# Kernel optimization log

Measured on AMD Instinct MI355X. Metric: run time of the kernel, lower is better.

## Reference

```python
import jax, jax.numpy as jnp
import numpy as np

N = 500_000       # nodes
E = 8_000_000     # edges (avg degree 16)
IN_DIM = 16       # node_in_dim
HID = 32          # DCRNN hidden (hard-coded in RecurrentGCN)
OUT_DIM = 8       # node_out_dim


def setup_inputs() -> dict:
    key = jax.random.key(0)
    ks = jax.random.split(key, 12)
    scale_g = 1.0 / np.sqrt(IN_DIM + HID)  # glorot-ish for DConv weights
    scale_l = 1.0 / np.sqrt(HID)
    return {
        "x": jax.random.normal(ks[0], (N, IN_DIM), jnp.float32),
        "edge_index": jax.random.randint(ks[1], (2, E), 0, N, jnp.int32),
        "edge_weight": jax.random.uniform(ks[2], (E,), jnp.float32),
        "h": jnp.zeros((N, HID), jnp.float32),
        # DConv weights: original shape (2, K=1, in, out); K=1 -> store (2, in, out)
        "w_z": jax.random.normal(ks[3], (2, IN_DIM + HID, HID), jnp.float32) * scale_g,
        "b_z": jnp.zeros((HID,), jnp.float32),
        "w_r": jax.random.normal(ks[4], (2, IN_DIM + HID, HID), jnp.float32) * scale_g,
        "b_r": jnp.zeros((HID,), jnp.float32),
        "w_h": jax.random.normal(ks[5], (2, IN_DIM + HID, HID), jnp.float32) * scale_g,
        "b_h": jnp.zeros((HID,), jnp.float32),
        "w_lin": jax.random.normal(ks[6], (HID, OUT_DIM), jnp.float32) * scale_l,
        "b_lin": jnp.zeros((OUT_DIM,), jnp.float32),
    }


def _dconv_k1(xh, w, b):
    # DConv with K=1: only the Chebyshev k=0 term survives:
    #   H = X @ W[0,0] + X @ W[1,0] + b  (out-diffusion + in-diffusion weights)
    # edge_index / edge_weight do not enter the math for K=1.
    return xh @ (w[0] + w[1]) + b


def reference(x, edge_index, edge_weight, h, w_z, b_z, w_r, b_r, w_h, b_h, w_lin, b_lin):
    # DCRNN GRU cell (h=None in torch -> zeros, supplied explicitly here)
    xh = jnp.concatenate([x, h], axis=1)                  # [N, IN+HID]
    z = jax.nn.sigmoid(_dconv_k1(xh, w_z, b_z))           # update gate [N, HID]
    r = jax.nn.sigmoid(_dconv_k1(xh, w_r, b_r))           # reset gate  [N, HID]
    xhr = jnp.concatenate([x, h * r], axis=1)             # [N, IN+HID]
    h_tilde = jnp.tanh(_dconv_k1(xhr, w_h, b_h))          # candidate   [N, HID]
    h_new = z * h + (1.0 - z) * h_tilde                   # [N, HID]
    out = jax.nn.relu(h_new) @ w_lin + b_lin              # [N, OUT_DIM]
    return (out, h_new)
```

## Files before the change

kernel.cpp:

```cpp
#include <hip/hip_runtime.h>


#define N_NODES 500000
#define IN_DIM  16
#define HID     32
#define OUT_DIM 8
#define XH      48
#define NTILES  31250
#define WROW    72

typedef unsigned int u32;
typedef unsigned short u16;
typedef __attribute__((ext_vector_type(8))) short bf16x8;
typedef __attribute__((ext_vector_type(4))) float f32x4;

static __device__ __forceinline__ float bfbits(u32 hi){ union{u32 x; float f;} t; t.x=hi; return t.f; }
static __device__ __forceinline__ float bflo(u32 u){ return bfbits(u<<16); }
static __device__ __forceinline__ float bfhi(u32 u){ return bfbits(u & 0xffff0000u); }
static __device__ __forceinline__ float bf2f(u16 s){ return bfbits(((u32)s)<<16); }
static __device__ __forceinline__ float u2f(u32 u){ union{u32 x; float f;} t; t.x=u; return t.f; }
static __device__ __forceinline__ u32 f2u(float f){ union{float f;u32 x;} t; t.f=f; return t.x; }
static __device__ __forceinline__ u32 cvtpk(float a, float b){
    u32 r; asm("v_cvt_pk_bf16_f32 %0, %1, %2" : "=v"(r) : "v"(a), "v"(b)); return r;
}
static __device__ __forceinline__ u16 f2bf(float f){
    union{float f;u32 x;} t; t.f=f; u32 x=t.x;
    return (u16)((x + 0x7fffu + ((x>>16)&1u)) >> 16);
}
static __device__ __forceinline__ float sigm(float a){
    return 1.f / (1.f + __expf(-a));
}
static __device__ __forceinline__ float tanh_(float a){
    float e = __expf(-2.f * fabsf(a));
    float t = (1.f - e) / (1.f + e);
    return __builtin_copysignf(t, a);
}

#define LFENCE() asm volatile("s_waitcnt lgkmcnt(0)" ::: "memory")
#define MFMA16(a,b,c) __builtin_amdgcn_mfma_f32_16x16x32_bf16(a,b,c,0,0,0)

static __device__ __forceinline__ float ldf(const void* p, int i, bool F32){
    return F32 ? ((const float*)p)[i] : bf2f(((const u16*)p)[i]);
}
static __device__ __forceinline__ float wsum(const void* wp, int k, int c, bool F32){
    int i0 = k*HID + c;
    return ldf(wp, i0, F32) + ldf(wp, XH*HID + i0, F32);
}
static __device__ __forceinline__ char* stgp(char* base, int row, int off){
    return base + row*128 + (off ^ ((row & 7) << 4));
}

__global__ __launch_bounds__(256)
void rgcn_kernel(const void* __restrict__ xp_,
                 const void* __restrict__ hp_,
                 const void* __restrict__ wz_, const void* __restrict__ bz_,
                 const void* __restrict__ wr_, const void* __restrict__ br_,
                 const void* __restrict__ wh_, const void* __restrict__ bh_,
                 const void* __restrict__ wl_, const void* __restrict__ bl_,
                 void* __restrict__ dout_)
{
    __shared__ u16 sW[3][32*WROW];
    __shared__ u16 sStage[4][16*64];
    __shared__ int sF32;

    const int tid = threadIdx.x;

    if (tid < 64) {
        const u32* xw = (const u32*)xp_;
        int bad = 0;
#pragma unroll
        for (int q = 0; q < 2; q++) {
            float lo = bflo(xw[tid*2 + q]);
            if (!(fabsf(lo) <= 1e6f)) bad = 1;
        }
        unsigned long long m = __ballot(bad);
        if (tid == 0) sF32 = (m != 0ull) ? 1 : 0;
    }
    __syncthreads();
    const bool F32 = (sF32 != 0);

    {
        const void* wsrc[3] = { wz_, wr_, wh_ };
#pragma unroll
        for (int m = 0; m < 3; m++) {
            u32* dst = (u32*)sW[m];
            for (int o = tid; o < 32*(WROW/2); o += 256) {
                int c = o / (WROW/2), kk = o - c*(WROW/2);
                int k0 = 2*kk, k1 = 2*kk + 1;
                float v0 = (k0 < XH) ? wsum(wsrc[m], k0, c, F32) : 0.f;
                float v1 = (k1 < XH) ? wsum(wsrc[m], k1, c, F32) : 0.f;
                dst[o] = cvtpk(v0, v1);
            }
        }
    }
    __syncthreads();

    const int lane = tid & 63, wv = tid >> 6;
    const int c16 = lane & 15, g = lane >> 4;
    const int row4 = lane >> 2, q4 = lane & 3;
    char* stage = (char*)sStage[wv];

    char* pXw = stgp(stage, row4, q4*8);
    char* pHw = stgp(stage, row4, 32 + q4*16);
    char* pA0 = stgp(stage, c16, 16*g);
    char* pA1 = stgp(stage, c16, 64 + 16*g);
    char* pPairH[4]; char* pPairR[4];
#pragma unroll
    for (int rr = 0; rr < 4; rr++) {
        int nl = g*4 + rr;
        pPairH[rr] = stgp(stage, nl, 32 + 4*c16);
        pPairR[rr] = stgp(stage, nl, 4*c16);
    }

    {
        uint2 z2; z2.x = 0u; z2.y = 0u;
        *(uint2*)stgp(stage, row4, 96 + q4*8) = z2;
    }

    float bzv[2], brv[2], bhv[2];
#pragma unroll
    for (int tt = 0; tt < 2; tt++) {
        bzv[tt] = ldf(bz_, 2*c16 + tt, F32);
        brv[tt] = ldf(br_, 2*c16 + tt, F32);
        bhv[tt] = ldf(bh_, 2*c16 + tt, F32);
    }
    float blv = (c16 < OUT_DIM) ? ldf(bl_, c16, F32) : 0.f;

    bf16x8 Bz[2][2], Br[2][2], Bh[2][2], Bl;
#pragma unroll
    for (int kt = 0; kt < 2; kt++) {
#pragma unroll
        for (int tt = 0; tt < 2; tt++) {
            int boff = (2*c16 + tt)*(WROW*2) + (kt*32 + g*8)*2;
            Bz[kt][tt] = *(const bf16x8*)((const char*)sW[0] + boff);
            Br[kt][tt] = *(const bf16x8*)((const char*)sW[1] + boff);
            Bh[kt][tt] = *(const bf16x8*)((const char*)sW[2] + boff);
        }
    }
    {
        union { u16 us[8]; bf16x8 v; } ul;
#pragma unroll
        for (int e = 0; e < 8; e++) {
            int k = g*8 + e;
            float v = (c16 < OUT_DIM) ? ldf(wl_, k*OUT_DIM + c16, F32) : 0.f;
            ul.us[e] = f2bf(v);
        }
        Bl = ul.v;
    }

    float* outF = (float*)dout_;
    float* hnF  = outF + (size_t)N_NODES * OUT_DIM;
    u16*   outB = (u16*)dout_;
    u16*   hnB  = outB + (size_t)N_NODES * OUT_DIM;

    const int wid = blockIdx.x*4 + wv;
    const int nw  = gridDim.x*4;

    float4 pfx, pfh0, pfh1;
#define PLOAD(TT) do { \
        size_t nbp = (size_t)(TT) * 16; \
        if (F32) { \
            const float* xb = (const float*)xp_ + nbp*IN_DIM; \
            pfx  = *(const float4*)(xb + row4*IN_DIM + q4*4); \
            const float* hb = (const float*)hp_ + nbp*HID; \
            pfh0 = *(const float4*)(hb + row4*HID + q4*8); \
            pfh1 = *(const float4*)(hb + row4*HID + q4*8 + 4); \
        } else { \
            const u16* xb = (const u16*)xp_ + nbp*IN_DIM; \
            uint2 xv = *(const uint2*)(xb + row4*IN_DIM + q4*4); \
            pfx.x = u2f(xv.x); pfx.y = u2f(xv.y); \
            const u16* hb = (const u16*)hp_ + nbp*HID; \
            uint4 hv = *(const uint4*)(hb + row4*HID + q4*8); \
            pfh0.x = u2f(hv.x); pfh0.y = u2f(hv.y); pfh0.z = u2f(hv.z); pfh0.w = u2f(hv.w); \
        } \
    } while (0)

    if (wid < NTILES) PLOAD(wid);

    for (int t = wid; t < NTILES; t += nw) {
        const size_t nb = (size_t)t * 16;

        if (F32) {
            uint2 xp2; xp2.x = cvtpk(pfx.x, pfx.y); xp2.y = cvtpk(pfx.z, pfx.w);
            *(uint2*)pXw = xp2;
            uint4 hp4; hp4.x = cvtpk(pfh0.x, pfh0.y); hp4.y = cvtpk(pfh0.z, pfh0.w);
            hp4.z = cvtpk(pfh1.x, pfh1.y); hp4.w = cvtpk(pfh1.z, pfh1.w);
            *(uint4*)pHw = hp4;
        } else {
            uint2 xp2; xp2.x = f2u(pfx.x); xp2.y = f2u(pfx.y);
            *(uint2*)pXw = xp2;
            uint4 hp4; hp4.x = f2u(pfh0.x); hp4.y = f2u(pfh0.y);
            hp4.z = f2u(pfh0.z); hp4.w = f2u(pfh0.w);
            *(uint4*)pHw = hp4;
        }

        {
            int tn = t + nw;
            if (tn < NTILES) PLOAD(tn);
        }
        LFENCE();

        bf16x8 a0 = *(const bf16x8*)pA0;
        bf16x8 a1 = *(const bf16x8*)pA1;
        u32 hwp[4];
#pragma unroll
        for (int rr = 0; rr < 4; rr++) hwp[rr] = *(const u32*)pPairH[rr];

        f32x4 accZ[2], accR[2];
#pragma unroll
        for (int tt = 0; tt < 2; tt++) {
            f32x4 az; az[0]=bzv[tt]; az[1]=bzv[tt]; az[2]=bzv[tt]; az[3]=bzv[tt];
            az = MFMA16(a0, Bz[0][tt], az);
            az = MFMA16(a1, Bz[1][tt], az);
            accZ[tt] = az;
            f32x4 ar; ar[0]=brv[tt]; ar[1]=brv[tt]; ar[2]=brv[tt]; ar[3]=brv[tt];
            ar = MFMA16(a0, Br[0][tt], ar);
            ar = MFMA16(a1, Br[1][tt], ar);
            accR[tt] = ar;
        }

        float z0a[4], z1a[4], hv0[4], hv1[4];
#pragma unroll
        for (int rr = 0; rr < 4; rr++) {
            float h0 = bflo(hwp[rr]), h1 = bfhi(hwp[rr]);
            hv0[rr] = h0; hv1[rr] = h1;
            float z0 = sigm(accZ[0][rr]), z1 = sigm(accZ[1][rr]);
            z0a[rr] = z0; z1a[rr] = z1;
            float r0 = sigm(accR[0][rr]), r1 = sigm(accR[1][rr]);
            *(u32*)pPairH[rr] = cvtpk(h0*r0, h1*r1);
        }
        LFENCE();

        bf16x8 b0 = *(const bf16x8*)pA0;
        bf16x8 b1 = *(const bf16x8*)pA1;
        f32x4 accH[2];
#pragma unroll
        for (int tt = 0; tt < 2; tt++) {
            f32x4 ah; ah[0]=bhv[tt]; ah[1]=bhv[tt]; ah[2]=bhv[tt]; ah[3]=bhv[tt];
            ah = MFMA16(b0, Bh[0][tt], ah);
            ah = MFMA16(b1, Bh[1][tt], ah);
            accH[tt] = ah;
        }

#pragma unroll
        for (int rr = 0; rr < 4; rr++) {
            int nl = g*4 + rr;
            float t0 = tanh_(accH[0][rr]), t1 = tanh_(accH[1][rr]);
            float n0 = t0 + z0a[rr]*(hv0[rr] - t0);
            float n1 = t1 + z1a[rr]*(hv1[rr] - t1);
            *(u32*)pPairR[rr] = cvtpk(fmaxf(n0, 0.f), fmaxf(n1, 0.f));
            if (F32) {
                float2 st; st.x = n0; st.y = n1;
                *(float2*)(hnF + (nb + nl)*HID + 2*c16) = st;
            } else {
                *(u32*)(hnB + (nb + nl)*HID + 2*c16) = cvtpk(n0, n1);
            }
        }
        LFENCE();

        bf16x8 a3 = *(const bf16x8*)pA0;
        f32x4 accO; accO[0]=blv; accO[1]=blv; accO[2]=blv; accO[3]=blv;
        accO = MFMA16(a3, Bl, accO);
        if (c16 < OUT_DIM) {
            if (F32) {
#pragma unroll
                for (int rr = 0; rr < 4; rr++)
                    outF[(nb + g*4 + rr)*OUT_DIM + c16] = accO[rr];
            } else {
#pragma unroll
                for (int rr = 0; rr < 4; rr++)
                    outB[(nb + g*4 + rr)*OUT_DIM + c16] = (u16)(cvtpk(accO[rr], accO[rr]) & 0xffffu);
            }
        }
    }
#undef PLOAD
}

extern "C" void kernel_launch(void* const* d_in, const int* in_sizes, int n_in,
                              void* d_out, int out_size, void* d_ws, size_t ws_size,
                              hipStream_t stream) {
    const int block = 256;
    const int grid  = 2048;
    rgcn_kernel<<<grid, block, 0, stream>>>(
        d_in[0], d_in[3], d_in[4], d_in[5], d_in[6], d_in[7],
        d_in[8], d_in[9], d_in[10], d_in[11], d_out);
}
```

Baseline: 252.5 us.

## Transpose MFMA operands to drop LDS staging and use ds_bpermute shuffles

Result: slower. 262.2 us (+3.8%).

```diff
diff --git a/kernel.cpp b/kernel.cpp
--- a/kernel.cpp
+++ b/kernel.cpp
@@ -18,8 +18,6 @@
 static __device__ __forceinline__ float bflo(u32 u){ return bfbits(u<<16); }
 static __device__ __forceinline__ float bfhi(u32 u){ return bfbits(u & 0xffff0000u); }
 static __device__ __forceinline__ float bf2f(u16 s){ return bfbits(((u32)s)<<16); }
-static __device__ __forceinline__ float u2f(u32 u){ union{u32 x; float f;} t; t.x=u; return t.f; }
-static __device__ __forceinline__ u32 f2u(float f){ union{float f;u32 x;} t; t.f=f; return t.x; }
 static __device__ __forceinline__ u32 cvtpk(float a, float b){
     u32 r; asm("v_cvt_pk_bf16_f32 %0, %1, %2" : "=v"(r) : "v"(a), "v"(b)); return r;
 }
@@ -27,17 +25,18 @@
     union{float f;u32 x;} t; t.f=f; u32 x=t.x;
     return (u16)((x + 0x7fffu + ((x>>16)&1u)) >> 16);
 }
+static __device__ __forceinline__ float rcp_(float x){
+    float r; asm("v_rcp_f32 %0, %1" : "=v"(r) : "v"(x)); return r;
+}
 static __device__ __forceinline__ float sigm(float a){
-    return 1.f / (1.f + __expf(-a));
+    return rcp_(1.f + __expf(-a));
 }
 static __device__ __forceinline__ float tanh_(float a){
     float e = __expf(-2.f * fabsf(a));
-    float t = (1.f - e) / (1.f + e);
-    return __builtin_copysignf(t, a);
-}
-
-#define LFENCE() asm volatile("s_waitcnt lgkmcnt(0)" ::: "memory")
+    return __builtin_copysignf((1.f - e) * rcp_(1.f + e), a);
+}
 #define MFMA16(a,b,c) __builtin_amdgcn_mfma_f32_16x16x32_bf16(a,b,c,0,0,0)
+#define BPERM(i,v)    ((u32)__builtin_amdgcn_ds_bpermute((int)(i),(int)(v)))
 
 static __device__ __forceinline__ float ldf(const void* p, int i, bool F32){
     return F32 ? ((const float*)p)[i] : bf2f(((const u16*)p)[i]);
@@ -45,9 +44,6 @@
 static __device__ __forceinline__ float wsum(const void* wp, int k, int c, bool F32){
     int i0 = k*HID + c;
     return ldf(wp, i0, F32) + ldf(wp, XH*HID + i0, F32);
-}
-static __device__ __forceinline__ char* stgp(char* base, int row, int off){
-    return base + row*128 + (off ^ ((row & 7) << 4));
 }
 
 __global__ __launch_bounds__(256)
@@ -60,7 +56,6 @@
                  void* __restrict__ dout_)
 {
     __shared__ u16 sW[3][32*WROW];
-    __shared__ u16 sStage[4][16*64];
     __shared__ int sF32;
 
     const int tid = threadIdx.x;
@@ -97,46 +92,37 @@
 
     const int lane = tid & 63, wv = tid >> 6;
     const int c16 = lane & 15, g = lane >> 4;
-    const int row4 = lane >> 2, q4 = lane & 3;
-    char* stage = (char*)sStage[wv];
-
-    char* pXw = stgp(stage, row4, q4*8);
-    char* pHw = stgp(stage, row4, 32 + q4*16);
-    char* pA0 = stgp(stage, c16, 16*g);
-    char* pA1 = stgp(stage, c16, 64 + 16*g);
-    char* pPairH[4]; char* pPairR[4];
+    const bool gLow = (g < 2);
+
+    const int idxA = (c16 + 32*(g & 1)) * 4;
+    const int idxB = idxA + 64;
+
+    float bzv[2][4], brv[2][4], bhv[2][4], blv[4];
+#pragma unroll
+    for (int jt = 0; jt < 2; jt++)
+#pragma unroll
+        for (int rr = 0; rr < 4; rr++) {
+            int j = jt*16 + g*4 + rr;
+            bzv[jt][rr] = ldf(bz_, j, F32);
+            brv[jt][rr] = ldf(br_, j, F32);
+            bhv[jt][rr] = ldf(bh_, j, F32);
+        }
 #pragma unroll
     for (int rr = 0; rr < 4; rr++) {
-        int nl = g*4 + rr;
-        pPairH[rr] = stgp(stage, nl, 32 + 4*c16);
-        pPairR[rr] = stgp(stage, nl, 4*c16);
-    }
-
-    {
-        uint2 z2; z2.x = 0u; z2.y = 0u;
-        *(uint2*)stgp(stage, row4, 96 + q4*8) = z2;
-    }
-
-    float bzv[2], brv[2], bhv[2];
-#pragma unroll
-    for (int tt = 0; tt < 2; tt++) {
-        bzv[tt] = ldf(bz_, 2*c16 + tt, F32);
-        brv[tt] = ldf(br_, 2*c16 + tt, F32);
-        bhv[tt] = ldf(bh_, 2*c16 + tt, F32);
-    }
-    float blv = (c16 < OUT_DIM) ? ldf(bl_, c16, F32) : 0.f;
-
-    bf16x8 Bz[2][2], Br[2][2], Bh[2][2], Bl;
-#pragma unroll
-    for (int kt = 0; kt < 2; kt++) {
-#pragma unroll
-        for (int tt = 0; tt < 2; tt++) {
-            int boff = (2*c16 + tt)*(WROW*2) + (kt*32 + g*8)*2;
-            Bz[kt][tt] = *(const bf16x8*)((const char*)sW[0] + boff);
-            Br[kt][tt] = *(const bf16x8*)((const char*)sW[1] + boff);
-            Bh[kt][tt] = *(const bf16x8*)((const char*)sW[2] + boff);
-        }
-    }
+        int o = g*4 + rr;
+        blv[rr] = (o < OUT_DIM) ? ldf(bl_, o, F32) : 0.f;
+    }
+
+    bf16x8 Az[2][2], Ar[2][2], Ah[2][2], Al;
+#pragma unroll
+    for (int jt = 0; jt < 2; jt++)
+#pragma unroll
+        for (int kt = 0; kt < 2; kt++) {
+            int off = (jt*16 + c16)*(WROW*2) + (kt*32 + g*8)*2;
+            Az[jt][kt] = *(const bf16x8*)((const char*)sW[0] + off);
+            Ar[jt][kt] = *(const bf16x8*)((const char*)sW[1] + off);
+            Ah[jt][kt] = *(const bf16x8*)((const char*)sW[2] + off);
+        }
     {
         union { u16 us[8]; bf16x8 v; } ul;
 #pragma unroll
@@ -145,7 +131,7 @@
             float v = (c16 < OUT_DIM) ? ldf(wl_, k*OUT_DIM + c16, F32) : 0.f;
             ul.us[e] = f2bf(v);
         }
-        Bl = ul.v;
+        Al = ul.v;
     }
 
     float* outF = (float*)dout_;
@@ -156,22 +142,29 @@
     const int wid = blockIdx.x*4 + wv;
     const int nw  = gridDim.x*4;
 
-    float4 pfx, pfh0, pfh1;
+    uint4 pk0a, pk0b, pk1a, pk1b, phv0, phv1;
 #define PLOAD(TT) do { \
-        size_t nbp = (size_t)(TT) * 16; \
+        size_t nr = (size_t)(TT)*16 + c16; \
         if (F32) { \
-            const float* xb = (const float*)xp_ + nbp*IN_DIM; \
-            pfx  = *(const float4*)(xb + row4*IN_DIM + q4*4); \
-            const float* hb = (const float*)hp_ + nbp*HID; \
-            pfh0 = *(const float4*)(hb + row4*HID + q4*8); \
-            pfh1 = *(const float4*)(hb + row4*HID + q4*8 + 4); \
+            const char* xr = (const char*)xp_ + nr*64; \
+            const char* hr = (const char*)hp_ + nr*128; \
+            const char* p0 = gLow ? (xr + g*32) : (hr + (g-2)*32); \
+            pk0a = *(const uint4*)p0; pk0b = *(const uint4*)(p0 + 16); \
+            if (gLow) { \
+                pk1a = *(const uint4*)(hr + 64 + g*32); \
+                pk1b = *(const uint4*)(hr + 80 + g*32); \
+            } \
+            phv0 = *(const uint4*)(hr + g*16); \
+            phv1 = *(const uint4*)(hr + 64 + g*16); \
         } else { \
-            const u16* xb = (const u16*)xp_ + nbp*IN_DIM; \
-            uint2 xv = *(const uint2*)(xb + row4*IN_DIM + q4*4); \
-            pfx.x = u2f(xv.x); pfx.y = u2f(xv.y); \
-            const u16* hb = (const u16*)hp_ + nbp*HID; \
-            uint4 hv = *(const uint4*)(hb + row4*HID + q4*8); \
-            pfh0.x = u2f(hv.x); pfh0.y = u2f(hv.y); pfh0.z = u2f(hv.z); pfh0.w = u2f(hv.w); \
+            const char* xr = (const char*)xp_ + nr*32; \
+            const char* hr = (const char*)hp_ + nr*64; \
+            const char* p0 = gLow ? (xr + g*16) : (hr + (g-2)*16); \
+            pk0a = *(const uint4*)p0; \
+            if (gLow) pk1a = *(const uint4*)(hr + 32 + g*16); \
+            uint2 a = *(const uint2*)(hr + g*8); \
+            uint2 b = *(const uint2*)(hr + 32 + g*8); \
+            phv0.x = a.x; phv0.y = a.y; phv1.x = b.x; phv1.y = b.y; \
         } \
     } while (0)
 
@@ -180,96 +173,127 @@
     for (int t = wid; t < NTILES; t += nw) {
         const size_t nb = (size_t)t * 16;
 
+        u32 f0w[4], f1w[4];
+        float hvf[8];
         if (F32) {
-            uint2 xp2; xp2.x = cvtpk(pfx.x, pfx.y); xp2.y = cvtpk(pfx.z, pfx.w);
-            *(uint2*)pXw = xp2;
-            uint4 hp4; hp4.x = cvtpk(pfh0.x, pfh0.y); hp4.y = cvtpk(pfh0.z, pfh0.w);
-            hp4.z = cvtpk(pfh1.x, pfh1.y); hp4.w = cvtpk(pfh1.z, pfh1.w);
-            *(uint4*)pHw = hp4;
+            f0w[0] = cvtpk(bfbits(0)+0.f, 0.f), f0w[0] = cvtpk(((const float*)&pk0a)[0], ((const float*)&pk0a)[1]);
+            f0w[1] = cvtpk(((const float*)&pk0a)[2], ((const float*)&pk0a)[3]);
+            f0w[2] = cvtpk(((const float*)&pk0b)[0], ((const float*)&pk0b)[1]);
+            f0w[3] = cvtpk(((const float*)&pk0b)[2], ((const float*)&pk0b)[3]);
+            f1w[0] = cvtpk(((const float*)&pk1a)[0], ((const float*)&pk1a)[1]);
+            f1w[1] = cvtpk(((const float*)&pk1a)[2], ((const float*)&pk1a)[3]);
+            f1w[2] = cvtpk(((const float*)&pk1b)[0], ((const float*)&pk1b)[1]);
+            f1w[3] = cvtpk(((const float*)&pk1b)[2], ((const float*)&pk1b)[3]);
+#pragma unroll
+            for (int q = 0; q < 4; q++) {
+                hvf[q]   = ((const float*)&phv0)[q];
+                hvf[4+q] = ((const float*)&phv1)[q];
+            }
         } else {
-            uint2 xp2; xp2.x = f2u(pfx.x); xp2.y = f2u(pfx.y);
-            *(uint2*)pXw = xp2;
-            uint4 hp4; hp4.x = f2u(pfh0.x); hp4.y = f2u(pfh0.y);
-            hp4.z = f2u(pfh0.z); hp4.w = f2u(pfh0.w);
-            *(uint4*)pHw = hp4;
-        }
-
-        {
-            int tn = t + nw;
-            if (tn < NTILES) PLOAD(tn);
-        }
-        LFENCE();
-
-        bf16x8 a0 = *(const bf16x8*)pA0;
-        bf16x8 a1 = *(const bf16x8*)pA1;
-        u32 hwp[4];
-#pragma unroll
-        for (int rr = 0; rr < 4; rr++) hwp[rr] = *(const u32*)pPairH[rr];
+            f0w[0] = pk0a.x; f0w[1] = pk0a.y; f0w[2] = pk0a.z; f0w[3] = pk0a.w;
+            f1w[0] = pk1a.x; f1w[1] = pk1a.y; f1w[2] = pk1a.z; f1w[3] = pk1a.w;
+            hvf[0] = bflo(phv0.x); hvf[1] = bfhi(phv0.x);
+            hvf[2] = bflo(phv0.y); hvf[3] = bfhi(phv0.y);
+            hvf[4] = bflo(phv1.x); hvf[5] = bfhi(phv1.x);
+            hvf[6] = bflo(phv1.y); hvf[7] = bfhi(phv1.y);
+        }
+        union { u32 w[4]; bf16x8 v; } uf0, uf1;
+#pragma unroll
+        for (int q = 0; q < 4; q++) {
+            uf0.w[q] = f0w[q];
+            uf1.w[q] = gLow ? f1w[q] : 0u;
+        }
+        bf16x8 Fk0 = uf0.v, Fk1 = uf1.v;
+
+        { int tn = t + nw; if (tn < NTILES) PLOAD(tn); }
 
         f32x4 accZ[2], accR[2];
 #pragma unroll
-        for (int tt = 0; tt < 2; tt++) {
-            f32x4 az; az[0]=bzv[tt]; az[1]=bzv[tt]; az[2]=bzv[tt]; az[3]=bzv[tt];
-            az = MFMA16(a0, Bz[0][tt], az);
-            az = MFMA16(a1, Bz[1][tt], az);
-            accZ[tt] = az;
-            f32x4 ar; ar[0]=brv[tt]; ar[1]=brv[tt]; ar[2]=brv[tt]; ar[3]=brv[tt];
-            ar = MFMA16(a0, Br[0][tt], ar);
-            ar = MFMA16(a1, Br[1][tt], ar);
-            accR[tt] = ar;
-        }
-
-        float z0a[4], z1a[4], hv0[4], hv1[4];
+        for (int jt = 0; jt < 2; jt++) {
+            f32x4 az; az[0]=bzv[jt][0]; az[1]=bzv[jt][1]; az[2]=bzv[jt][2]; az[3]=bzv[jt][3];
+            az = MFMA16(Az[jt][0], Fk0, az);
+            az = MFMA16(Az[jt][1], Fk1, az);
+            accZ[jt] = az;
+            f32x4 ar; ar[0]=brv[jt][0]; ar[1]=brv[jt][1]; ar[2]=brv[jt][2]; ar[3]=brv[jt][3];
+            ar = MFMA16(Ar[jt][0], Fk0, ar);
+            ar = MFMA16(Ar[jt][1], Fk1, ar);
+            accR[jt] = ar;
+        }
+
+        float zv[2][4];
+        float hr0[4], hr1[4];
 #pragma unroll
         for (int rr = 0; rr < 4; rr++) {
-            float h0 = bflo(hwp[rr]), h1 = bfhi(hwp[rr]);
-            hv0[rr] = h0; hv1[rr] = h1;
-            float z0 = sigm(accZ[0][rr]), z1 = sigm(accZ[1][rr]);
-            z0a[rr] = z0; z1a[rr] = z1;
-            float r0 = sigm(accR[0][rr]), r1 = sigm(accR[1][rr]);
-            *(u32*)pPairH[rr] = cvtpk(h0*r0, h1*r1);
-        }
-        LFENCE();
-
-        bf16x8 b0 = *(const bf16x8*)pA0;
-        bf16x8 b1 = *(const bf16x8*)pA1;
+            zv[0][rr] = sigm(accZ[0][rr]);
+            zv[1][rr] = sigm(accZ[1][rr]);
+            hr0[rr] = hvf[rr]     * sigm(accR[0][rr]);
+            hr1[rr] = hvf[4+rr]   * sigm(accR[1][rr]);
+        }
+        u32 P0 = cvtpk(hr0[0], hr0[1]), P1 = cvtpk(hr0[2], hr0[3]);
+        u32 Q0 = cvtpk(hr1[0], hr1[1]), Q1 = cvtpk(hr1[2], hr1[3]);
+
+        u32 qa0 = BPERM(idxA, Q0), pa0 = BPERM(idxA, P0);
+        u32 qa1 = BPERM(idxA, Q1), pa1 = BPERM(idxA, P1);
+        u32 qb0 = BPERM(idxB, Q0), pb0 = BPERM(idxB, P0);
+        u32 qb1 = BPERM(idxB, Q1), pb1 = BPERM(idxB, P1);
+        u32 W0 = gLow ? qa0 : pa0, W1 = gLow ? qa1 : pa1;
+        u32 W2 = gLow ? qb0 : pb0, W3 = gLow ? qb1 : pb1;
+
+        union { u32 w[4]; bf16x8 v; } ub0, ub1;
+        ub0.w[0] = gLow ? f0w[0] : W0; ub0.w[1] = gLow ? f0w[1] : W1;
+        ub0.w[2] = gLow ? f0w[2] : W2; ub0.w[3] = gLow ? f0w[3] : W3;
+        ub1.w[0] = gLow ? W0 : 0u;     ub1.w[1] = gLow ? W1 : 0u;
+        ub1.w[2] = gLow ? W2 : 0u;     ub1.w[3] = gLow ? W3 : 0u;
+        bf16x8 B2k0 = ub0.v, B2k1 = ub1.v;
+
         f32x4 accH[2];
 #pragma unroll
-        for (int tt = 0; tt < 2; tt++) {
-            f32x4 ah; ah[0]=bhv[tt]; ah[1]=bhv[tt]; ah[2]=bhv[tt]; ah[3]=bhv[tt];
-            ah = MFMA16(b0, Bh[0][tt], ah);
-            ah = MFMA16(b1, Bh[1][tt], ah);
-            accH[tt] = ah;
-        }
-
-#pragma unroll
-        for (int rr = 0; rr < 4; rr++) {
-            int nl = g*4 + rr;
-            float t0 = tanh_(accH[0][rr]), t1 = tanh_(accH[1][rr]);
-            float n0 = t0 + z0a[rr]*(hv0[rr] - t0);
-            float n1 = t1 + z1a[rr]*(hv1[rr] - t1);
-            *(u32*)pPairR[rr] = cvtpk(fmaxf(n0, 0.f), fmaxf(n1, 0.f));
+        for (int jt = 0; jt < 2; jt++) {
+            f32x4 ah; ah[0]=bhv[jt][0]; ah[1]=bhv[jt][1]; ah[2]=bhv[jt][2]; ah[3]=bhv[jt][3];
+            ah = MFMA16(Ah[jt][0], B2k0, ah);
+            ah = MFMA16(Ah[jt][1], B2k1, ah);
+            accH[jt] = ah;
+        }
+
+        float rl0[4], rl1[4];
+#pragma unroll
+        for (int jt = 0; jt < 2; jt++) {
+            float n0 = tanh_(accH[jt][0]); n0 = n0 + zv[jt][0]*(hvf[jt*4+0] - n0);
+            float n1 = tanh_(accH[jt][1]); n1 = n1 + zv[jt][1]*(hvf[jt*4+1] - n1);
+            float n2 = tanh_(accH[jt][2]); n2 = n2 + zv[jt][2]*(hvf[jt*4+2] - n2);
+            float n3 = tanh_(accH[jt][3]); n3 = n3 + zv[jt][3]*(hvf[jt*4+3] - n3);
             if (F32) {
-                float2 st; st.x = n0; st.y = n1;
-                *(float2*)(hnF + (nb + nl)*HID + 2*c16) = st;
+                float4 st; st.x=n0; st.y=n1; st.z=n2; st.w=n3;
+                *(float4*)(hnF + (nb + c16)*HID + jt*16 + g*4) = st;
             } else {
-                *(u32*)(hnB + (nb + nl)*HID + 2*c16) = cvtpk(n0, n1);
+                uint2 st; st.x = cvtpk(n0, n1); st.y = cvtpk(n2, n3);
+                *(uint2*)(hnB + (nb + c16)*HID + jt*16 + g*4) = st;
             }
-        }
-        LFENCE();
-
-        bf16x8 a3 = *(const bf16x8*)pA0;
-        f32x4 accO; accO[0]=blv; accO[1]=blv; accO[2]=blv; accO[3]=blv;
-        accO = MFMA16(a3, Bl, accO);
-        if (c16 < OUT_DIM) {
+            float* rl = jt ? rl1 : rl0;
+            rl[0] = fmaxf(n0, 0.f); rl[1] = fmaxf(n1, 0.f);
+            rl[2] = fmaxf(n2, 0.f); rl[3] = fmaxf(n3, 0.f);
+        }
+        u32 RP0 = cvtpk(rl0[0], rl0[1]), RP1 = cvtpk(rl0[2], rl0[3]);
+        u32 RQ0 = cvtpk(rl1[0], rl1[1]), RQ1 = cvtpk(rl1[2], rl1[3]);
+
+        u32 rpa0 = BPERM(idxA, RP0), rqa0 = BPERM(idxA, RQ0);
+        u32 rpa1 = BPERM(idxA, RP1), rqa1 = BPERM(idxA, RQ1);
+        u32 rpb0 = BPERM(idxB, RP0), rqb0 = BPERM(idxB, RQ0);
+        u32 rpb1 = BPERM(idxB, RP1), rqb1 = BPERM(idxB, RQ1);
+        union { u32 w[4]; bf16x8 v; } ub3;
+        ub3.w[0] = gLow ? rpa0 : rqa0; ub3.w[1] = gLow ? rpa1 : rqa1;
+        ub3.w[2] = gLow ? rpb0 : rqb0; ub3.w[3] = gLow ? rpb1 : rqb1;
+        bf16x8 B3 = ub3.v;
+
+        f32x4 accO; accO[0]=blv[0]; accO[1]=blv[1]; accO[2]=blv[2]; accO[3]=blv[3];
+        accO = MFMA16(Al, B3, accO);
+        if (gLow) {
             if (F32) {
-#pragma unroll
-                for (int rr = 0; rr < 4; rr++)
-                    outF[(nb + g*4 + rr)*OUT_DIM + c16] = accO[rr];
+                float4 st; st.x=accO[0]; st.y=accO[1]; st.z=accO[2]; st.w=accO[3];
+                *(float4*)(outF + (nb + c16)*OUT_DIM + g*4) = st;
             } else {
-#pragma unroll
-                for (int rr = 0; rr < 4; rr++)
-                    outB[(nb + g*4 + rr)*OUT_DIM + c16] = (u16)(cvtpk(accO[rr], accO[rr]) & 0xffffu);
+                uint2 st; st.x = cvtpk(accO[0], accO[1]); st.y = cvtpk(accO[2], accO[3]);
+                *(uint2*)(outB + (nb + c16)*OUT_DIM + g*4) = st;
             }
         }
     }
```
